# Optimization experiments

Hardware: AMD Instinct MI355X
Metric: run time of the kernel (lower is better)

Reference implementation:

```python
import jax, jax.numpy as jnp
import numpy as np

N = 50000
E = 800000
IN_DIM = 128
HID = 64
OUT_DIM = 128
NEG_SLOPE = 0.2  # PyG GATConv default


def _add_self_loops(src, dst, edge_attr, n):
    # PyG GATConv(add_self_loops=True) with edge_dim uses fill_value='mean':
    # self-loop edge_attr = mean of edge_attr of incoming edges per node.
    deg = jax.ops.segment_sum(jnp.ones((src.shape[0],), edge_attr.dtype), dst, num_segments=n)
    loop_attr = jax.ops.segment_sum(edge_attr, dst, num_segments=n) / jnp.maximum(deg, 1.0)[:, None]
    loop = jnp.arange(n, dtype=src.dtype)
    return (jnp.concatenate([src, loop]), jnp.concatenate([dst, loop]),
            jnp.concatenate([edge_attr, loop_attr], axis=0))


def _gat_conv(x, src, dst, edge_attr, W, We, a_src, a_dst, a_edge, bias, heads, out_dim, concat, n):
    src, dst, edge_attr = _add_self_loops(src, dst, edge_attr, n)
    h = (x @ W).reshape(n, heads, out_dim)                      # [N,H,D]
    he = (edge_attr @ We).reshape(-1, heads, out_dim)           # [E',H,D]
    alpha_src = jnp.einsum('nhd,hd->nh', h, a_src)
    alpha_dst = jnp.einsum('nhd,hd->nh', h, a_dst)
    alpha_edge = jnp.einsum('ehd,hd->eh', he, a_edge)
    alpha = jax.nn.leaky_relu(alpha_src[src] + alpha_dst[dst] + alpha_edge, NEG_SLOPE)  # [E',H]
    # segment softmax over edges grouped by destination node
    amax = jax.ops.segment_max(alpha, dst, num_segments=n)
    amax = jnp.where(jnp.isfinite(amax), amax, 0.0)
    ex = jnp.exp(alpha - amax[dst])
    denom = jax.ops.segment_sum(ex, dst, num_segments=n)
    coef = ex / (denom[dst] + 1e-16)                            # [E',H]
    msg = h[src] * coef[:, :, None]                             # [E',H,D]
    out = jax.ops.segment_sum(msg, dst, num_segments=n)         # [N,H,D]
    out = out.reshape(n, heads * out_dim) if concat else out.mean(axis=1)
    return out + bias


def setup_inputs() -> dict:
    key = jax.random.key(0)
    ks = jax.random.split(key, 16)
    s = 0.05
    inp = {
        'x': jax.random.normal(ks[0], (N, IN_DIM), jnp.float32),
        'edge_index': jax.random.randint(ks[1], (2, E), 0, N, dtype=jnp.int64),
        'edge_attr': jax.random.normal(ks[2], (E, 2), jnp.float32),
        # gat1: heads=4, concat -> out 4*HID
        'W1': jax.random.normal(ks[3], (IN_DIM, 4 * HID), jnp.float32) * s,
        'We1': jax.random.normal(ks[4], (2, 4 * HID), jnp.float32) * s,
        'asrc1': jax.random.normal(ks[5], (4, HID), jnp.float32) * s,
        'adst1': jax.random.normal(ks[6], (4, HID), jnp.float32) * s,
        'aedge1': jax.random.normal(ks[7], (4, HID), jnp.float32) * s,
        'b1': jnp.zeros((4 * HID,), jnp.float32),
        # gat2: heads=1, concat=False -> out OUT_DIM
        'W2': jax.random.normal(ks[8], (4 * HID, OUT_DIM), jnp.float32) * s,
        'We2': jax.random.normal(ks[9], (2, OUT_DIM), jnp.float32) * s,
        'asrc2': jax.random.normal(ks[10], (1, OUT_DIM), jnp.float32) * s,
        'adst2': jax.random.normal(ks[11], (1, OUT_DIM), jnp.float32) * s,
        'aedge2': jax.random.normal(ks[12], (1, OUT_DIM), jnp.float32) * s,
        'b2': jnp.zeros((OUT_DIM,), jnp.float32),
    }
    return inp


def reference(x, edge_index, edge_attr, W1, We1, asrc1, adst1, aedge1, b1,
              W2, We2, asrc2, adst2, aedge2, b2):
    src, dst = edge_index[0], edge_index[1]
    # dropout layers are identity in eval mode
    h = _gat_conv(x, src, dst, edge_attr, W1, We1, asrc1, adst1, aedge1, b1,
                  heads=4, out_dim=HID, concat=True, n=x.shape[0])
    h = jax.nn.elu(h)
    out = _gat_conv(h, src, dst, edge_attr, W2, We2, asrc2, adst2, aedge2, b2,
                    heads=1, out_dim=OUT_DIM, concat=False, n=x.shape[0])
    return out
```

## Files before the change

kernel.cpp:

```cpp
#include <hip/hip_runtime.h>
#include <hip/hip_bf16.h>

#define NN 50000
#define EE 800000
#define SCAN_B 2048
#define NB ((NN + SCAN_B - 1) / SCAN_B)


typedef short bf16x8 __attribute__((ext_vector_type(8)));
typedef float f32x4  __attribute__((ext_vector_type(4)));

__device__ __forceinline__ float bf2f(unsigned short u) {
    return __uint_as_float(((unsigned)u) << 16);
}
__device__ __forceinline__ unsigned short f2bf(float f) {
    unsigned b = __float_as_uint(f);
    b += 0x7fffu + ((b >> 16) & 1u);
    return (unsigned short)(b >> 16);
}
__device__ __forceinline__ float2 bfpair(unsigned u) {
    return make_float2(__uint_as_float(u << 16), __uint_as_float(u & 0xffff0000u));
}

__global__ void k_prep(const float* __restrict__ We1, const float* __restrict__ ae1,
                       const float* __restrict__ We2, const float* __restrict__ ae2,
                       float* __restrict__ v,
                       const float* __restrict__ W1, unsigned short* __restrict__ W1t,
                       const float* __restrict__ W2, unsigned short* __restrict__ W2t,
                       const int* __restrict__ ei, int* __restrict__ idg,
                       int* __restrict__ rank,
                       const float* __restrict__ x, unsigned short* __restrict__ xb) {
    int bid = blockIdx.x, t = threadIdx.x;
    if (bid == 0) {
        if (t < 8) {
            int c = t >> 2, h = t & 3;
            float s = 0.f;
            for (int d = 0; d < 64; d++) s += We1[c * 256 + h * 64 + d] * ae1[h * 64 + d];
            v[c * 4 + h] = s;
        } else if (t < 10) {
            int c = t - 8;
            float s = 0.f;
            for (int d = 0; d < 128; d++) s += We2[c * 128 + d] * ae2[d];
            v[8 + c] = s;
        }
    } else if (bid <= 256) {
        int idx = (bid - 1) * 256 + t;
        if (idx < 32768) {
            int k = idx >> 8, n = idx & 255;
            W1t[n * 128 + k] = f2bf(W1[idx]);
        } else {
            int i = idx - 32768;
            int k = i >> 7, n = i & 127;
            W2t[n * 256 + k] = f2bf(W2[i]);
        }
    } else if (bid <= 256 + 3125) {
        int e = (bid - 257) * 256 + t;
        if (e < EE) rank[e] = atomicAdd(&idg[ei[EE + e]], 1);
    } else {
        int i = (bid - 3382) * 256 + t;
        if (i < NN * 128 / 4) {
            float4 vv = ((const float4*)x)[i];
            ushort4 o;
            o.x = f2bf(vv.x); o.y = f2bf(vv.y); o.z = f2bf(vv.z); o.w = f2bf(vv.w);
            ((ushort4*)xb)[i] = o;
        }
    }
}

__global__ void k_scan1(const int* __restrict__ idg, int* __restrict__ rowptr,
                        int* __restrict__ bsum) {
    __shared__ int sh[512];
    int t = threadIdx.x;
    int base = blockIdx.x * SCAN_B + t * 4;
    int v[4]; int s = 0;
    #pragma unroll
    for (int j = 0; j < 4; j++) {
        int i = base + j;
        v[j] = (i < NN) ? idg[i] : 0;
        s += v[j];
    }
    sh[t] = s;
    __syncthreads();
    for (int off = 1; off < 512; off <<= 1) {
        int a = (t >= off) ? sh[t - off] : 0;
        __syncthreads();
        sh[t] += a;
        __syncthreads();
    }
    int run = sh[t] - s;
    #pragma unroll
    for (int j = 0; j < 4; j++) {
        int i = base + j;
        if (i < NN) rowptr[i] = run;
        run += v[j];
    }
    if (t == 511) bsum[blockIdx.x] = sh[511];
}

__global__ void k_scan2(const int* __restrict__ bsum, int* __restrict__ boff,
                        int* __restrict__ rowptr) {
    if (threadIdx.x == 0) {
        int acc = 0;
        for (int b = 0; b < NB; b++) { boff[b] = acc; acc += bsum[b]; }
        rowptr[NN] = acc;
    }
}

__global__ void k_scan3(int* __restrict__ rowptr, const int* __restrict__ boff) {
    int t = threadIdx.x;
    int i = blockIdx.x * SCAN_B + t * 4;
    int off = boff[blockIdx.x];
    #pragma unroll
    for (int j = 0; j < 4; j++)
        if (i + j < NN) rowptr[i + j] += off;
}

__global__ void k_scatter(const int* __restrict__ ei, const float* __restrict__ eattr,
                          const int* __restrict__ rowptr, const int* __restrict__ rank,
                          int2* __restrict__ slot) {
    int e = blockIdx.x * blockDim.x + threadIdx.x;
    if (e >= EE) return;
    int s = ei[e], d = ei[EE + e];
    int p = rowptr[d] + rank[e];
    float2 a = ((const float2*)eattr)[e];
    unsigned a0 = f2bf(a.x), a1 = f2bf(a.y);
    slot[p] = make_int2(s, (int)(a0 | (a1 << 16)));
}

template <int K, int NT, int H>
__global__ __launch_bounds__(256) void gemm_mfma(const unsigned short* __restrict__ A,
                                                 const unsigned short* __restrict__ Bt,
                                                 unsigned short* __restrict__ C,
                                                 const float* __restrict__ avs,
                                                 const float* __restrict__ avd,
                                                 float* __restrict__ asrc,
                                                 float* __restrict__ adst,
                                                 int M, int N) {
    int wave = threadIdx.x >> 6, lane = threadIdx.x & 63;
    int l16 = lane & 15, quad = lane >> 4;
    int m0 = blockIdx.y * 128 + wave * 32;
    int n0 = blockIdx.x * (NT * 16);

    f32x4 acc[2][NT];
    #pragma unroll
    for (int mt = 0; mt < 2; mt++)
        #pragma unroll
        for (int nt = 0; nt < NT; nt++)
            acc[mt][nt] = (f32x4){0.f, 0.f, 0.f, 0.f};

    int ar0 = min(m0 + l16, M - 1);
    int ar1 = min(m0 + 16 + l16, M - 1);
    const unsigned short* a0 = A + (size_t)ar0 * K + quad * 8;
    const unsigned short* a1 = A + (size_t)ar1 * K + quad * 8;
    const unsigned short* bp = Bt + (size_t)(n0 + l16) * K + quad * 8;

    #pragma unroll
    for (int k0 = 0; k0 < K; k0 += 32) {
        bf16x8 af0 = *(const bf16x8*)(a0 + k0);
        bf16x8 af1 = *(const bf16x8*)(a1 + k0);
        #pragma unroll
        for (int nt = 0; nt < NT; nt++) {
            bf16x8 bf = *(const bf16x8*)(bp + (size_t)nt * 16 * K + k0);
            acc[0][nt] = __builtin_amdgcn_mfma_f32_16x16x32_bf16(af0, bf, acc[0][nt], 0, 0, 0);
            acc[1][nt] = __builtin_amdgcn_mfma_f32_16x16x32_bf16(af1, bf, acc[1][nt], 0, 0, 0);
        }
    }

    #pragma unroll
    for (int mt = 0; mt < 2; mt++)
        #pragma unroll
        for (int reg = 0; reg < 4; reg++) {
            int row = m0 + mt * 16 + quad * 4 + reg;
            if (row < M) {
                #pragma unroll
                for (int nt = 0; nt < NT; nt++)
                    C[(size_t)row * N + n0 + nt * 16 + l16] = f2bf(acc[mt][nt][reg]);
            }
        }

    float ws[NT], wd[NT];
    #pragma unroll
    for (int nt = 0; nt < NT; nt++) {
        ws[nt] = avs[n0 + nt * 16 + l16];
        wd[nt] = avd[n0 + nt * 16 + l16];
    }
    int hh = n0 >> 6;
    #pragma unroll
    for (int mt = 0; mt < 2; mt++)
        #pragma unroll
        for (int reg = 0; reg < 4; reg++) {
            int row = m0 + mt * 16 + quad * 4 + reg;
            float s1 = 0.f, s2 = 0.f;
            #pragma unroll
            for (int nt = 0; nt < NT; nt++) {
                float c = acc[mt][nt][reg];
                s1 += c * ws[nt];
                s2 += c * wd[nt];
            }
            #pragma unroll
            for (int off = 1; off < 16; off <<= 1) {
                s1 += __shfl_xor(s1, off);
                s2 += __shfl_xor(s2, off);
            }
            if (l16 == 0 && row < M) {
                asrc[row * H + hh] = s1;
                adst[row * H + hh] = s2;
            }
        }
}

__global__ __launch_bounds__(256) void k_agg1(const int* __restrict__ rowptr,
                       const int2* __restrict__ slot, const float* __restrict__ asrc,
                       const float* __restrict__ adst, const float* __restrict__ v,
                       const unsigned short* __restrict__ hb, const float* __restrict__ b1,
                       unsigned short* __restrict__ h2b) {
    int node = blockIdx.x * 4 + (threadIdx.x >> 6);
    if (node >= NN) return;
    int lane = threadIdx.x & 63;
    int j    = lane & 15;
    int hp   = lane >> 4;
    int half = lane >> 5;
    int hl   = lane & 31;
    int hh2  = hl >> 3;
    int beg = rowptr[node], end = rowptr[node + 1];
    float ad_p = adst[node * 4 + hp];
    float v0 = v[hp], v1 = v[4 + hp];
    float2 acc2[4] = {};
    float den = 0.f, s0 = 0.f, s1 = 0.f;

    int pb = beg;
    int m = min(16, end - pb);
    int sj = 0; float aa0 = 0.f, aa1 = 0.f, av = 0.f;
    if (j < m) {
        int2 sl = slot[pb + j];
        sj = sl.x;
        float2 a = bfpair((unsigned)sl.y);
        aa0 = a.x; aa1 = a.y;
        av = asrc[sj * 4 + hp];
    }
    while (pb < end) {
        int cm = m, csj = sj;
        float ca0 = aa0, ca1 = aa1, cav = av;
        pb += 16;
        m = min(16, end - pb);
        sj = 0; aa0 = 0.f; aa1 = 0.f; av = 0.f;
        if (j < m) {
            int2 sl = slot[pb + j];
            sj = sl.x;
            float2 a = bfpair((unsigned)sl.y);
            aa0 = a.x; aa1 = a.y;
            av = asrc[sj * 4 + hp];
        }
        float exv = 0.f;
        if (j < cm) {
            s0 += ca0; s1 += ca1;
            float al = cav + ad_p + ca0 * v0 + ca1 * v1;
            al = (al > 0.f) ? al : 0.2f * al;
            exv = __expf(al);
        }
        den += exv;
        #pragma unroll 2
        for (int j2 = 0; j2 < cm; j2 += 2) {
            int jj = j2 + half;
            int s   = __shfl(csj, jj);
            float w = __shfl(exv, jj + (hh2 << 4));
            uint4 raw = *(const uint4*)(hb + (size_t)s * 256 + hl * 8);
            float2 p0 = bfpair(raw.x), p1 = bfpair(raw.y);
            float2 p2 = bfpair(raw.z), p3 = bfpair(raw.w);
            acc2[0].x += w * p0.x; acc2[0].y += w * p0.y;
            acc2[1].x += w * p1.x; acc2[1].y += w * p1.y;
            acc2[2].x += w * p2.x; acc2[2].y += w * p2.y;
            acc2[3].x += w * p3.x; acc2[3].y += w * p3.y;
        }
    }
    #pragma unroll
    for (int off = 1; off < 16; off <<= 1) {
        s0 += __shfl_xor(s0, off);
        s1 += __shfl_xor(s1, off);
    }
    float dg = fmaxf((float)(end - beg), 1.0f);
    float als = asrc[node * 4 + hp] + ad_p + (s0 / dg) * v0 + (s1 / dg) * v1;
    als = (als > 0.f) ? als : 0.2f * als;
    float exs = __expf(als);
    #pragma unroll
    for (int off = 8; off; off >>= 1) den += __shfl_xor(den, off);
    den += exs;
    float den_h  = __shfl(den, hh2 << 4);
    float w_self = __shfl(exs, hh2 << 4);
    if (half == 0) {
        uint4 raw = *(const uint4*)(hb + (size_t)node * 256 + hl * 8);
        float2 p0 = bfpair(raw.x), p1 = bfpair(raw.y);
        float2 p2 = bfpair(raw.z), p3 = bfpair(raw.w);
        acc2[0].x += w_self * p0.x; acc2[0].y += w_self * p0.y;
        acc2[1].x += w_self * p1.x; acc2[1].y += w_self * p1.y;
        acc2[2].x += w_self * p2.x; acc2[2].y += w_self * p2.y;
        acc2[3].x += w_self * p3.x; acc2[3].y += w_self * p3.y;
    }
    #pragma unroll
    for (int k = 0; k < 4; k++) {
        acc2[k].x += __shfl_down(acc2[k].x, 32);
        acc2[k].y += __shfl_down(acc2[k].y, 32);
    }
    if (lane < 32) {
        float inv = 1.f / (den_h + 1e-16f);
        short ov[8];
        #pragma unroll
        for (int k = 0; k < 4; k++) {
            float va = acc2[k].x * inv + b1[hl * 8 + 2 * k];
            float vb = acc2[k].y * inv + b1[hl * 8 + 2 * k + 1];
            va = (va > 0.f) ? va : __expf(va) - 1.f;
            vb = (vb > 0.f) ? vb : __expf(vb) - 1.f;
            ov[2 * k]     = (short)f2bf(va);
            ov[2 * k + 1] = (short)f2bf(vb);
        }
        bf16x8 o = {ov[0], ov[1], ov[2], ov[3], ov[4], ov[5], ov[6], ov[7]};
        *(bf16x8*)(h2b + (size_t)node * 256 + hl * 8) = o;
    }
}

__global__ __launch_bounds__(256) void k_agg2(const int* __restrict__ rowptr,
                       const int2* __restrict__ slot, const float* __restrict__ asrc,
                       const float* __restrict__ adst, const float* __restrict__ v,
                       const unsigned short* __restrict__ gb, const float* __restrict__ b2,
                       float* __restrict__ outp) {
    int node = blockIdx.x * 4 + (threadIdx.x >> 6);
    if (node >= NN) return;
    int lane = threadIdx.x & 63;
    int q  = lane >> 4;
    int ql = lane & 15;
    int beg = rowptr[node], end = rowptr[node + 1];
    float ad = adst[node];
    float v0 = v[0], v1 = v[1];
    float2 acc2[4] = {};
    float den = 0.f, s0 = 0.f, s1 = 0.f;
    for (int pb = beg; pb < end; pb += 64) {
        int m = min(64, end - pb);
        int sj = 0; float exv = 0.f;
        if (lane < m) {
            int2 sl = slot[pb + lane];
            sj = sl.x;
            float2 a = bfpair((unsigned)sl.y);
            s0 += a.x; s1 += a.y;
            float al = asrc[sj] + ad + a.x * v0 + a.y * v1;
            al = (al > 0.f) ? al : 0.2f * al;
            exv = __expf(al);
        }
        den += exv;
        #pragma unroll 2
        for (int j2 = 0; j2 < m; j2 += 4) {
            int jj = j2 + q;
            int s   = __shfl(sj, jj);
            float w = __shfl(exv, jj);
            uint4 raw = *(const uint4*)(gb + (size_t)s * 128 + ql * 8);
            float2 p0 = bfpair(raw.x), p1 = bfpair(raw.y);
            float2 p2 = bfpair(raw.z), p3 = bfpair(raw.w);
            acc2[0].x += w * p0.x; acc2[0].y += w * p0.y;
            acc2[1].x += w * p1.x; acc2[1].y += w * p1.y;
            acc2[2].x += w * p2.x; acc2[2].y += w * p2.y;
            acc2[3].x += w * p3.x; acc2[3].y += w * p3.y;
        }
    }
    #pragma unroll
    for (int off = 32; off; off >>= 1) {
        s0  += __shfl_xor(s0, off);
        s1  += __shfl_xor(s1, off);
        den += __shfl_xor(den, off);
    }
    float dg = fmaxf((float)(end - beg), 1.0f);
    float als = asrc[node] + ad + (s0 / dg) * v0 + (s1 / dg) * v1;
    als = (als > 0.f) ? als : 0.2f * als;
    float exs = __expf(als);
    den += exs;
    if (q == 0) {
        uint4 raw = *(const uint4*)(gb + (size_t)node * 128 + ql * 8);
        float2 p0 = bfpair(raw.x), p1 = bfpair(raw.y);
        float2 p2 = bfpair(raw.z), p3 = bfpair(raw.w);
        acc2[0].x += exs * p0.x; acc2[0].y += exs * p0.y;
        acc2[1].x += exs * p1.x; acc2[1].y += exs * p1.y;
        acc2[2].x += exs * p2.x; acc2[2].y += exs * p2.y;
        acc2[3].x += exs * p3.x; acc2[3].y += exs * p3.y;
    }
    #pragma unroll
    for (int k = 0; k < 4; k++) {
        acc2[k].x += __shfl_down(acc2[k].x, 32);
        acc2[k].y += __shfl_down(acc2[k].y, 32);
        acc2[k].x += __shfl_down(acc2[k].x, 16);
        acc2[k].y += __shfl_down(acc2[k].y, 16);
    }
    if (lane < 16) {
        float inv = 1.f / (den + 1e-16f);
        float4 o0, o1;
        o0.x = acc2[0].x * inv + b2[ql * 8 + 0];
        o0.y = acc2[0].y * inv + b2[ql * 8 + 1];
        o0.z = acc2[1].x * inv + b2[ql * 8 + 2];
        o0.w = acc2[1].y * inv + b2[ql * 8 + 3];
        o1.x = acc2[2].x * inv + b2[ql * 8 + 4];
        o1.y = acc2[2].y * inv + b2[ql * 8 + 5];
        o1.z = acc2[3].x * inv + b2[ql * 8 + 6];
        o1.w = acc2[3].y * inv + b2[ql * 8 + 7];
        *(float4*)(outp + (size_t)node * 128 + ql * 8)     = o0;
        *(float4*)(outp + (size_t)node * 128 + ql * 8 + 4) = o1;
    }
}

extern "C" void kernel_launch(void* const* d_in, const int* in_sizes, int n_in,
                              void* d_out, int out_size, void* d_ws, size_t ws_size,
                              hipStream_t stream) {
    const float* x     = (const float*)d_in[0];
    const int*   ei    = (const int*)d_in[1];
    const float* eattr = (const float*)d_in[2];
    const float* W1    = (const float*)d_in[3];
    const float* We1   = (const float*)d_in[4];
    const float* as1   = (const float*)d_in[5];
    const float* ad1   = (const float*)d_in[6];
    const float* ae1   = (const float*)d_in[7];
    const float* b1    = (const float*)d_in[8];
    const float* W2    = (const float*)d_in[9];
    const float* We2   = (const float*)d_in[10];
    const float* as2   = (const float*)d_in[11];
    const float* ad2   = (const float*)d_in[12];
    const float* ae2   = (const float*)d_in[13];
    const float* b2    = (const float*)d_in[14];
    float* out = (float*)d_out;

    int* idg    = (int*)d_ws;
    int* rank   = idg + NN;
    int* rowptr = rank + EE;
    int* bsum   = rowptr + NN + 16;
    int* boff   = bsum + 32;
    int2* slot  = (int2*)(boff + 32);
    float* asrc1 = (float*)(slot + EE);
    float* adst1 = asrc1 + 4 * NN;
    float* asrc2 = adst1 + 4 * NN;
    float* adst2 = asrc2 + NN;
    float* vbuf  = adst2 + NN;
    unsigned short* ub = (unsigned short*)(((uintptr_t)(vbuf + 64) + 63) & ~(uintptr_t)63);
    unsigned short* x_bf  = ub;
    unsigned short* W1t   = x_bf + (size_t)NN * 128;
    unsigned short* W2t   = W1t + 32768;
    unsigned short* h1_bf = W2t + 32768;
    unsigned short* h2_bf = h1_bf + (size_t)NN * 256;
    unsigned short* g2_bf = h2_bf + (size_t)NN * 256;

    hipMemsetAsync(idg, 0, (size_t)NN * sizeof(int), stream);

    k_prep<<<9632, 256, 0, stream>>>(We1, ae1, We2, ae2, vbuf, W1, W1t, W2, W2t,
                                     ei, idg, rank, x, x_bf);
    k_scan1<<<NB, 512, 0, stream>>>(idg, rowptr, bsum);
    k_scan2<<<1, 64, 0, stream>>>(bsum, boff, rowptr);
    k_scan3<<<NB, 512, 0, stream>>>(rowptr, boff);
    k_scatter<<<(EE + 255) / 256, 256, 0, stream>>>(ei, eattr, rowptr, rank, slot);

    gemm_mfma<128, 4, 4><<<dim3(4, (NN + 127) / 128), 256, 0, stream>>>(
        x_bf, W1t, h1_bf, as1, ad1, asrc1, adst1, NN, 256);
    k_agg1<<<(NN + 3) / 4, 256, 0, stream>>>(rowptr, slot, asrc1, adst1, vbuf,
                                             h1_bf, b1, h2_bf);

    gemm_mfma<256, 8, 1><<<dim3(1, (NN + 127) / 128), 256, 0, stream>>>(
        h2_bf, W2t, g2_bf, as2, ad2, asrc2, adst2, NN, 128);
    k_agg2<<<(NN + 3) / 4, 256, 0, stream>>>(rowptr, slot, asrc2, adst2, vbuf + 8,
                                             g2_bf, b2, out);
}
```

Measured before the change: 337.2 us.

## Restructure GAT aggregation so each lane computes its own edge weights without shuffles

Both aggregation kernels now split the wave into four quarter-groups, each handling one edge at a time. Every lane loads the slot, attention source scores and feature row for its own edge and computes the softmax weight locally, instead of computing weights cooperatively and broadcasting them with shuffles. In layer 1 each lane covers two heads with 16 floats of accumulators. This removes the per-edge shuffle and batching overhead, but it recomputes the exp redundantly across the 16 lanes of a group and raises register pressure.

```diff
diff --git a/kernel.cpp b/kernel.cpp
--- a/kernel.cpp
+++ b/kernel.cpp
@@ -217,104 +217,99 @@
     int node = blockIdx.x * 4 + (threadIdx.x >> 6);
     if (node >= NN) return;
     int lane = threadIdx.x & 63;
-    int j    = lane & 15;
-    int hp   = lane >> 4;
-    int half = lane >> 5;
-    int hl   = lane & 31;
-    int hh2  = hl >> 3;
+    int q  = lane >> 4;
+    int ql = lane & 15;
+    int hA = ql >> 3;
+    int hB = hA + 2;
     int beg = rowptr[node], end = rowptr[node + 1];
-    float ad_p = adst[node * 4 + hp];
-    float v0 = v[hp], v1 = v[4 + hp];
-    float2 acc2[4] = {};
-    float den = 0.f, s0 = 0.f, s1 = 0.f;
+    float pdA = adst[node * 4 + hA], pdB = adst[node * 4 + hB];
+    float vA0 = v[hA],     vA1 = v[4 + hA];
+    float vB0 = v[hB],     vB1 = v[4 + hB];
+    float accA[8] = {}, accB[8] = {};
+    float denA = 0.f, denB = 0.f, s0 = 0.f, s1 = 0.f;
+    const unsigned short* hbq = hb + ql * 8;
+
+    auto edge = [&](int jj) {
+        int2 sl = slot[jj];
+        int s = sl.x;
+        float2 a = bfpair((unsigned)sl.y);
+        float psA = asrc[s * 4 + hA];
+        float psB = asrc[s * 4 + hB];
+        float alA = psA + pdA + a.x * vA0 + a.y * vA1;
+        float alB = psB + pdB + a.x * vB0 + a.y * vB1;
+        alA = (alA > 0.f) ? alA : 0.2f * alA;
+        alB = (alB > 0.f) ? alB : 0.2f * alB;
+        float eA = __expf(alA), eB = __expf(alB);
+        s0 += a.x; s1 += a.y;
+        denA += eA; denB += eB;
+        const uint4* rp = (const uint4*)(hbq + (size_t)s * 256);
+        uint4 r0 = rp[0];
+        uint4 r1 = rp[16];
+        float2 p;
+        p = bfpair(r0.x); accA[0] += eA * p.x; accA[1] += eA * p.y;
+        p = bfpair(r0.y); accA[2] += eA * p.x; accA[3] += eA * p.y;
+        p = bfpair(r0.z); accA[4] += eA * p.x; accA[5] += eA * p.y;
+        p = bfpair(r0.w); accA[6] += eA * p.x; accA[7] += eA * p.y;
+        p = bfpair(r1.x); accB[0] += eB * p.x; accB[1] += eB * p.y;
+        p = bfpair(r1.y); accB[2] += eB * p.x; accB[3] += eB * p.y;
+        p = bfpair(r1.z); accB[4] += eB * p.x; accB[5] += eB * p.y;
+        p = bfpair(r1.w); accB[6] += eB * p.x; accB[7] += eB * p.y;
+    };
 
     int pb = beg;
-    int m = min(16, end - pb);
-    int sj = 0; float aa0 = 0.f, aa1 = 0.f, av = 0.f;
-    if (j < m) {
-        int2 sl = slot[pb + j];
-        sj = sl.x;
-        float2 a = bfpair((unsigned)sl.y);
-        aa0 = a.x; aa1 = a.y;
-        av = asrc[sj * 4 + hp];
-    }
-    while (pb < end) {
-        int cm = m, csj = sj;
-        float ca0 = aa0, ca1 = aa1, cav = av;
-        pb += 16;
-        m = min(16, end - pb);
-        sj = 0; aa0 = 0.f; aa1 = 0.f; av = 0.f;
-        if (j < m) {
-            int2 sl = slot[pb + j];
-            sj = sl.x;
-            float2 a = bfpair((unsigned)sl.y);
-            aa0 = a.x; aa1 = a.y;
-            av = asrc[sj * 4 + hp];
-        }
-        float exv = 0.f;
-        if (j < cm) {
-            s0 += ca0; s1 += ca1;
-            float al = cav + ad_p + ca0 * v0 + ca1 * v1;
-            al = (al > 0.f) ? al : 0.2f * al;
-            exv = __expf(al);
-        }
-        den += exv;
-        #pragma unroll 2
-        for (int j2 = 0; j2 < cm; j2 += 2) {
-            int jj = j2 + half;
-            int s   = __shfl(csj, jj);
-            float w = __shfl(exv, jj + (hh2 << 4));
-            uint4 raw = *(const uint4*)(hb + (size_t)s * 256 + hl * 8);
-            float2 p0 = bfpair(raw.x), p1 = bfpair(raw.y);
-            float2 p2 = bfpair(raw.z), p3 = bfpair(raw.w);
-            acc2[0].x += w * p0.x; acc2[0].y += w * p0.y;
-            acc2[1].x += w * p1.x; acc2[1].y += w * p1.y;
-            acc2[2].x += w * p2.x; acc2[2].y += w * p2.y;
-            acc2[3].x += w * p3.x; acc2[3].y += w * p3.y;
-        }
-    }
-    #pragma unroll
-    for (int off = 1; off < 16; off <<= 1) {
-        s0 += __shfl_xor(s0, off);
-        s1 += __shfl_xor(s1, off);
-    }
+    int mend = end - ((end - beg) & 3);
+    #pragma unroll 2
+    for (; pb < mend; pb += 4) edge(pb + q);
+    if (pb + q < end) edge(pb + q);
+
+    #pragma unroll
+    for (int k = 0; k < 8; k++) {
+        accA[k] += __shfl_down(accA[k], 32);
+        accB[k] += __shfl_down(accB[k], 32);
+        accA[k] += __shfl_down(accA[k], 16);
+        accB[k] += __shfl_down(accB[k], 16);
+    }
+    denA += __shfl_xor(denA, 16); denA += __shfl_xor(denA, 32);
+    denB += __shfl_xor(denB, 16); denB += __shfl_xor(denB, 32);
+    s0   += __shfl_xor(s0, 16);   s0   += __shfl_xor(s0, 32);
+    s1   += __shfl_xor(s1, 16);   s1   += __shfl_xor(s1, 32);
+
     float dg = fmaxf((float)(end - beg), 1.0f);
-    float als = asrc[node * 4 + hp] + ad_p + (s0 / dg) * v0 + (s1 / dg) * v1;
-    als = (als > 0.f) ? als : 0.2f * als;
-    float exs = __expf(als);
-    #pragma unroll
-    for (int off = 8; off; off >>= 1) den += __shfl_xor(den, off);
-    den += exs;
-    float den_h  = __shfl(den, hh2 << 4);
-    float w_self = __shfl(exs, hh2 << 4);
-    if (half == 0) {
-        uint4 raw = *(const uint4*)(hb + (size_t)node * 256 + hl * 8);
-        float2 p0 = bfpair(raw.x), p1 = bfpair(raw.y);
-        float2 p2 = bfpair(raw.z), p3 = bfpair(raw.w);
-        acc2[0].x += w_self * p0.x; acc2[0].y += w_self * p0.y;
-        acc2[1].x += w_self * p1.x; acc2[1].y += w_self * p1.y;
-        acc2[2].x += w_self * p2.x; acc2[2].y += w_self * p2.y;
-        acc2[3].x += w_self * p3.x; acc2[3].y += w_self * p3.y;
-    }
-    #pragma unroll
-    for (int k = 0; k < 4; k++) {
-        acc2[k].x += __shfl_down(acc2[k].x, 32);
-        acc2[k].y += __shfl_down(acc2[k].y, 32);
-    }
-    if (lane < 32) {
-        float inv = 1.f / (den_h + 1e-16f);
-        short ov[8];
+    float alsA = asrc[node * 4 + hA] + pdA + (s0 / dg) * vA0 + (s1 / dg) * vA1;
+    float alsB = asrc[node * 4 + hB] + pdB + (s0 / dg) * vB0 + (s1 / dg) * vB1;
+    alsA = (alsA > 0.f) ? alsA : 0.2f * alsA;
+    alsB = (alsB > 0.f) ? alsB : 0.2f * alsB;
+    float exA = __expf(alsA), exB = __expf(alsB);
+    denA += exA; denB += exB;
+
+    if (q == 0) {
+        const uint4* rp = (const uint4*)(hbq + (size_t)node * 256);
+        uint4 r0 = rp[0], r1 = rp[16];
+        float2 p;
+        p = bfpair(r0.x); accA[0] += exA * p.x; accA[1] += exA * p.y;
+        p = bfpair(r0.y); accA[2] += exA * p.x; accA[3] += exA * p.y;
+        p = bfpair(r0.z); accA[4] += exA * p.x; accA[5] += exA * p.y;
+        p = bfpair(r0.w); accA[6] += exA * p.x; accA[7] += exA * p.y;
+        p = bfpair(r1.x); accB[0] += exB * p.x; accB[1] += exB * p.y;
+        p = bfpair(r1.y); accB[2] += exB * p.x; accB[3] += exB * p.y;
+        p = bfpair(r1.z); accB[4] += exB * p.x; accB[5] += exB * p.y;
+        p = bfpair(r1.w); accB[6] += exB * p.x; accB[7] += exB * p.y;
+        float invA = 1.f / (denA + 1e-16f);
+        float invB = 1.f / (denB + 1e-16f);
+        short oa[8], ob[8];
         #pragma unroll
-        for (int k = 0; k < 4; k++) {
-            float va = acc2[k].x * inv + b1[hl * 8 + 2 * k];
-            float vb = acc2[k].y * inv + b1[hl * 8 + 2 * k + 1];
+        for (int k = 0; k < 8; k++) {
+            float va = accA[k] * invA + b1[ql * 8 + k];
+            float vb = accB[k] * invB + b1[128 + ql * 8 + k];
             va = (va > 0.f) ? va : __expf(va) - 1.f;
             vb = (vb > 0.f) ? vb : __expf(vb) - 1.f;
-            ov[2 * k]     = (short)f2bf(va);
-            ov[2 * k + 1] = (short)f2bf(vb);
-        }
-        bf16x8 o = {ov[0], ov[1], ov[2], ov[3], ov[4], ov[5], ov[6], ov[7]};
-        *(bf16x8*)(h2b + (size_t)node * 256 + hl * 8) = o;
+            oa[k] = (short)f2bf(va);
+            ob[k] = (short)f2bf(vb);
+        }
+        bf16x8 vA8 = {oa[0], oa[1], oa[2], oa[3], oa[4], oa[5], oa[6], oa[7]};
+        bf16x8 vB8 = {ob[0], ob[1], ob[2], ob[3], ob[4], ob[5], ob[6], ob[7]};
+        *(bf16x8*)(h2b + (size_t)node * 256 + ql * 8)       = vA8;
+        *(bf16x8*)(h2b + (size_t)node * 256 + 128 + ql * 8) = vB8;
     }
 }
 
@@ -331,73 +326,64 @@
     int beg = rowptr[node], end = rowptr[node + 1];
     float ad = adst[node];
     float v0 = v[0], v1 = v[1];
-    float2 acc2[4] = {};
+    float acc[8] = {};
     float den = 0.f, s0 = 0.f, s1 = 0.f;
-    for (int pb = beg; pb < end; pb += 64) {
-        int m = min(64, end - pb);
-        int sj = 0; float exv = 0.f;
-        if (lane < m) {
-            int2 sl = slot[pb + lane];
-            sj = sl.x;
-            float2 a = bfpair((unsigned)sl.y);
-            s0 += a.x; s1 += a.y;
-            float al = asrc[sj] + ad + a.x * v0 + a.y * v1;
-            al = (al > 0.f) ? al : 0.2f * al;
-            exv = __expf(al);
-        }
-        den += exv;
-        #pragma unroll 2
-        for (int j2 = 0; j2 < m; j2 += 4) {
-            int jj = j2 + q;
-            int s   = __shfl(sj, jj);
-            float w = __shfl(exv, jj);
-            uint4 raw = *(const uint4*)(gb + (size_t)s * 128 + ql * 8);
-            float2 p0 = bfpair(raw.x), p1 = bfpair(raw.y);
-            float2 p2 = bfpair(raw.z), p3 = bfpair(raw.w);
-            acc2[0].x += w * p0.x; acc2[0].y += w * p0.y;
-            acc2[1].x += w * p1.x; acc2[1].y += w * p1.y;
-            acc2[2].x += w * p2.x; acc2[2].y += w * p2.y;
-            acc2[3].x += w * p3.x; acc2[3].y += w * p3.y;
-        }
-    }
-    #pragma unroll
-    for (int off = 32; off; off >>= 1) {
-        s0  += __shfl_xor(s0, off);
-        s1  += __shfl_xor(s1, off);
-        den += __shfl_xor(den, off);
-    }
+    const unsigned short* gbq = gb + ql * 8;
+
+    auto edge = [&](int jj) {
+        int2 sl = slot[jj];
+        int s = sl.x;
+        float2 a = bfpair((unsigned)sl.y);
+        float al = asrc[s] + ad + a.x * v0 + a.y * v1;
+        al = (al > 0.f) ? al : 0.2f * al;
+        float e = __expf(al);
+        s0 += a.x; s1 += a.y; den += e;
+        uint4 r = *(const uint4*)(gbq + (size_t)s * 128);
+        float2 p;
+        p = bfpair(r.x); acc[0] += e * p.x; acc[1] += e * p.y;
+        p = bfpair(r.y); acc[2] += e * p.x; acc[3] += e * p.y;
+        p = bfpair(r.z); acc[4] += e * p.x; acc[5] += e * p.y;
+        p = bfpair(r.w); acc[6] += e * p.x; acc[7] += e * p.y;
+    };
+
+    int pb = beg;
+    int mend = end - ((end - beg) & 3);
+    #pragma unroll 2
+    for (; pb < mend; pb += 4) edge(pb + q);
+    if (pb + q < end) edge(pb + q);
+
+    #pragma unroll
+    for (int k = 0; k < 8; k++) {
+        acc[k] += __shfl_down(acc[k], 32);
+        acc[k] += __shfl_down(acc[k], 16);
+    }
+    den += __shfl_xor(den, 16); den += __shfl_xor(den, 32);
+    s0  += __shfl_xor(s0, 16);  s0  += __shfl_xor(s0, 32);
+    s1  += __shfl_xor(s1, 16);  s1  += __shfl_xor(s1, 32);
+
     float dg = fmaxf((float)(end - beg), 1.0f);
     float als = asrc[node] + ad + (s0 / dg) * v0 + (s1 / dg) * v1;
     als = (als > 0.f) ? als : 0.2f * als;
     float exs = __expf(als);
     den += exs;
+
     if (q == 0) {
-        uint4 raw = *(const uint4*)(gb + (size_t)node * 128 + ql * 8);
-        float2 p0 = bfpair(raw.x), p1 = bfpair(raw.y);
-        float2 p2 = bfpair(raw.z), p3 = bfpair(raw.w);
-        acc2[0].x += exs * p0.x; acc2[0].y += exs * p0.y;
-        acc2[1].x += exs * p1.x; acc2[1].y += exs * p1.y;
-        acc2[2].x += exs * p2.x; acc2[2].y += exs * p2.y;
-        acc2[3].x += exs * p3.x; acc2[3].y += exs * p3.y;
-    }
-    #pragma unroll
-    for (int k = 0; k < 4; k++) {
-        acc2[k].x += __shfl_down(acc2[k].x, 32);
-        acc2[k].y += __shfl_down(acc2[k].y, 32);
-        acc2[k].x += __shfl_down(acc2[k].x, 16);
-        acc2[k].y += __shfl_down(acc2[k].y, 16);
-    }
-    if (lane < 16) {
+        uint4 r = *(const uint4*)(gbq + (size_t)node * 128);
+        float2 p;
+        p = bfpair(r.x); acc[0] += exs * p.x; acc[1] += exs * p.y;
+        p = bfpair(r.y); acc[2] += exs * p.x; acc[3] += exs * p.y;
+        p = bfpair(r.z); acc[4] += exs * p.x; acc[5] += exs * p.y;
+        p = bfpair(r.w); acc[6] += exs * p.x; acc[7] += exs * p.y;
         float inv = 1.f / (den + 1e-16f);
         float4 o0, o1;
-        o0.x = acc2[0].x * inv + b2[ql * 8 + 0];
-        o0.y = acc2[0].y * inv + b2[ql * 8 + 1];
-        o0.z = acc2[1].x * inv + b2[ql * 8 + 2];
-        o0.w = acc2[1].y * inv + b2[ql * 8 + 3];
-        o1.x = acc2[2].x * inv + b2[ql * 8 + 4];
-        o1.y = acc2[2].y * inv + b2[ql * 8 + 5];
-        o1.z = acc2[3].x * inv + b2[ql * 8 + 6];
-        o1.w = acc2[3].y * inv + b2[ql * 8 + 7];
+        o0.x = acc[0] * inv + b2[ql * 8 + 0];
+        o0.y = acc[1] * inv + b2[ql * 8 + 1];
+        o0.z = acc[2] * inv + b2[ql * 8 + 2];
+        o0.w = acc[3] * inv + b2[ql * 8 + 3];
+        o1.x = acc[4] * inv + b2[ql * 8 + 4];
+        o1.y = acc[5] * inv + b2[ql * 8 + 5];
+        o1.z = acc[6] * inv + b2[ql * 8 + 6];
+        o1.w = acc[7] * inv + b2[ql * 8 + 7];
         *(float4*)(outp + (size_t)node * 128 + ql * 8)     = o0;
         *(float4*)(outp + (size_t)node * 128 + ql * 8 + 4) = o1;
     }
```

New measurement: 339.6 us. About the same (+0.7%).
